# Performance work log

Measured on AMD Instinct MI355X. Metric: run time of the kernel, lower is better.

## Reference

```python
import jax, jax.numpy as jnp
import numpy as np

B, MBITS, P = 4096, 64, 64
BLK = P // 8          # 8: block size for crop-robust pattern
FREQ = P // 4         # 16: low-res frequency pattern size
KS, SIGMA = 5, 1.0


def _interp_matrix(n_in, n_out):
    # 1D bilinear interpolation matrix with align_corners=True semantics
    pos = jnp.arange(n_out, dtype=jnp.float32) * (n_in - 1) / (n_out - 1)
    lo = jnp.floor(pos).astype(jnp.int32)
    hi = jnp.minimum(lo + 1, n_in - 1)
    w = pos - lo.astype(jnp.float32)
    rows = jnp.arange(n_out)
    M = jnp.zeros((n_out, n_in), jnp.float32)
    M = M.at[rows, lo].add(1.0 - w).at[rows, hi].add(w)
    return M


def _gaussian_kernel(ks, sigma):
    c = jnp.arange(ks, dtype=jnp.float32) - ks // 2
    g = jnp.exp(-c**2 / (2.0 * sigma**2))
    g = g / g.sum()
    k2 = jnp.outer(g, g)
    return k2 / k2.sum()


def setup_inputs() -> dict:
    key = jax.random.key(0)
    ks = jax.random.split(key, 8)

    def lin(k, fan_in, fan_out):
        lim = 1.0 / np.sqrt(fan_in)
        return jax.random.uniform(k, (fan_in, fan_out), jnp.float32, -lim, lim)

    return {
        'message': jax.random.uniform(ks[0], (B, MBITS), jnp.float32),
        'sW1': lin(ks[1], MBITS, 256), 'sb1': jnp.zeros((256,), jnp.float32),
        'sW2': lin(ks[2], 256, 512),   'sb2': jnp.zeros((512,), jnp.float32),
        'sW3': lin(ks[3], 512, P * P), 'sb3': jnp.zeros((P * P,), jnp.float32),
        'fW1': lin(ks[4], MBITS, 128), 'fb1': jnp.zeros((128,), jnp.float32),
        'fW2': lin(ks[5], 128, FREQ * FREQ), 'fb2': jnp.zeros((FREQ * FREQ,), jnp.float32),
    }


def reference(message, sW1, sb1, sW2, sb2, sW3, sb3, fW1, fb1, fW2, fb2):
    b = message.shape[0]
    # --- spatial pattern: MLP -> tanh -> [B,1,P,P]
    h = jax.nn.relu(message @ sW1 + sb1)
    h = jax.nn.relu(h @ sW2 + sb2)
    spatial = jnp.tanh(h @ sW3 + sb3).reshape(b, 1, P, P)

    # --- frequency pattern: MLP -> tanh -> [B,1,16,16] -> bilinear upsample to PxP
    f = jax.nn.relu(message @ fW1 + fb1)
    freq_lo = jnp.tanh(f @ fW2 + fb2).reshape(b, FREQ, FREQ)
    M = _interp_matrix(FREQ, P)  # [P, FREQ]
    freq = jnp.einsum('ph,bhw,qw->bpq', M, freq_lo, M)[:, None]  # [B,1,P,P]

    # --- block pattern: bit i -> 8x8 block (row-major over an 8x8 grid)
    blocks = message.reshape(b, 8, 8)  # [B, rows, cols] of bits
    block = jnp.repeat(jnp.repeat(blocks, BLK, axis=1), BLK, axis=2)[:, None]  # [B,1,P,P]

    rgb = jnp.concatenate([spatial, freq, block], axis=1)  # [B,3,P,P]

    # --- depthwise 5x5 Gaussian smoothing, groups=3
    k2 = _gaussian_kernel(KS, SIGMA)
    kernel = jnp.broadcast_to(k2, (3, 1, KS, KS))
    out = jax.lax.conv_general_dilated(
        rgb, kernel, window_strides=(1, 1), padding=[(KS // 2, KS // 2)] * 2,
        dimension_numbers=('NCHW', 'OIHW', 'NCHW'), feature_group_count=3)
    return out
```

## Files before the change

kernel.cpp:

```cpp
#include <hip/hip_runtime.h>
#include <math.h>

#define BATCH 4096

typedef __attribute__((ext_vector_type(8))) short short8;
typedef __attribute__((ext_vector_type(4))) float f32x4;

__device__ __forceinline__ unsigned short f2bf(float f) {
  unsigned int u = __float_as_uint(f);
  u += 0x7FFF + ((u >> 16) & 1);
  return (unsigned short)(u >> 16);
}

__device__ __forceinline__ float bf2f(unsigned short s) {
  return __uint_as_float(((unsigned int)s) << 16);
}

__device__ __forceinline__ float fast_tanh(float x) {
  const float e = __expf(2.0f * x);
  const float r = __builtin_amdgcn_rcpf(e + 1.0f);
  return fmaf(-2.0f, r, 1.0f);
}

#define GLL16(g, l)                                                    \
  __builtin_amdgcn_global_load_lds(                                    \
      (const __attribute__((address_space(1))) unsigned int*)(g),      \
      (__attribute__((address_space(3))) unsigned int*)(l), 16, 0, 0)

__global__ __launch_bounds__(256) void prep_kernel(
    const float* __restrict__ sW1, const float* __restrict__ sW2,
    const float* __restrict__ sW3, const float* __restrict__ msg,
    unsigned short* __restrict__ w1T, unsigned short* __restrict__ w2T,
    unsigned short* __restrict__ w3T, unsigned short* __restrict__ msgb) {
  const int b = blockIdx.x;
  const int t = threadIdx.x;

  if (b >= 2192) {
    const int i0 = (b - 2192) * 2048 + t * 8;
    const float4 v0 = *reinterpret_cast<const float4*>(&msg[i0]);
    const float4 v1 = *reinterpret_cast<const float4*>(&msg[i0 + 4]);
    short8 o;
    o[0] = (short)f2bf(v0.x); o[1] = (short)f2bf(v0.y);
    o[2] = (short)f2bf(v0.z); o[3] = (short)f2bf(v0.w);
    o[4] = (short)f2bf(v1.x); o[5] = (short)f2bf(v1.y);
    o[6] = (short)f2bf(v1.z); o[7] = (short)f2bf(v1.w);
    *reinterpret_cast<short8*>(&msgb[i0]) = o;
    return;
  }

  const float* src;
  unsigned short* dst;
  int K, N, lgtN, tile;
  if (b < 16) {
    src = sW1; dst = w1T; K = 64; N = 256; lgtN = 3; tile = b;
  } else if (b < 144) {
    src = sW2; dst = w2T; K = 256; N = 512; lgtN = 4; tile = b - 16;
  } else {
    src = sW3; dst = w3T; K = 512; N = 4096; lgtN = 7; tile = b - 144;
  }
  const int ty = tile >> lgtN;
  const int tx = tile & ((1 << lgtN) - 1);

  __shared__ float tl[32][33];
  {
    const int r = t >> 3, c4 = (t & 7) * 4;
    const float4 v =
        *reinterpret_cast<const float4*>(&src[(size_t)(ty * 32 + r) * N + tx * 32 + c4]);
    tl[r][c4 + 0] = v.x; tl[r][c4 + 1] = v.y;
    tl[r][c4 + 2] = v.z; tl[r][c4 + 3] = v.w;
  }
  __syncthreads();
  {
    const int nl = t >> 3, k4 = (t & 7) * 4;
    unsigned short o[4];
#pragma unroll
    for (int i = 0; i < 4; ++i) o[i] = f2bf(tl[k4 + i][nl]);
    *reinterpret_cast<ushort4*>(&dst[(size_t)(tx * 32 + nl) * K + ty * 32 + k4]) =
        *reinterpret_cast<const ushort4*>(o);
  }
}

template <int ACT, int OBF16, int KDIM>
__global__ __launch_bounds__(256) void gemm_mfma(
    const unsigned short* __restrict__ A, const unsigned short* __restrict__ BT,
    const float* __restrict__ bias, void* __restrict__ Cv, int ldc) {
  __shared__ __align__(16) unsigned short As[128 * 32];
  __shared__ __align__(16) unsigned short Bs[128 * 32];

  const int t = threadIdx.x;
  const int lane = t & 63;
  const int w = t >> 6;
  const int bm = blockIdx.x * 128;
  const int bn = blockIdx.y * 128;

  const int r0 = w * 32 + (lane >> 2);
  const int r1 = r0 + 16;
  const int c0 = (lane & 3) ^ ((r0 >> 1) & 3);
  const int c1 = (lane & 3) ^ ((r1 >> 1) & 3);

  const unsigned short* gA0 = A + (size_t)(bm + r0) * KDIM + c0 * 8;
  const unsigned short* gA1 = A + (size_t)(bm + r1) * KDIM + c1 * 8;
  const unsigned short* gB0 = BT + (size_t)(bn + r0) * KDIM + c0 * 8;
  const unsigned short* gB1 = BT + (size_t)(bn + r1) * KDIM + c1 * 8;

  unsigned short* lA0 = &As[(w * 2 + 0) * 512];
  unsigned short* lA1 = &As[(w * 2 + 1) * 512];
  unsigned short* lB0 = &Bs[(w * 2 + 0) * 512];
  unsigned short* lB1 = &Bs[(w * 2 + 1) * 512];

  const int wm = (w >> 1) * 64;
  const int wn = (w & 1) * 64;
  const int lr = lane & 15;
  const int lc = lane >> 4;
  int aoff[4], boff[4];
#pragma unroll
  for (int i = 0; i < 4; ++i) {
    const int row = wm + i * 16 + lr;
    aoff[i] = row * 32 + (lc ^ ((row >> 1) & 3)) * 8;
    const int col = wn + i * 16 + lr;
    boff[i] = col * 32 + (lc ^ ((col >> 1) & 3)) * 8;
  }

  f32x4 acc[4][4];
  const f32x4 z = {0.f, 0.f, 0.f, 0.f};
#pragma unroll
  for (int i = 0; i < 4; ++i)
#pragma unroll
    for (int j = 0; j < 4; ++j) acc[i][j] = z;

#pragma unroll 1
  for (int kt = 0; kt < KDIM / 32; ++kt) {
    GLL16(gA0, lA0);
    GLL16(gA1, lA1);
    GLL16(gB0, lB0);
    GLL16(gB1, lB1);
    __syncthreads();

    short8 a[4], b[4];
#pragma unroll
    for (int i = 0; i < 4; ++i) a[i] = *reinterpret_cast<const short8*>(&As[aoff[i]]);
#pragma unroll
    for (int j = 0; j < 4; ++j) b[j] = *reinterpret_cast<const short8*>(&Bs[boff[j]]);

#pragma unroll
    for (int i = 0; i < 4; ++i)
#pragma unroll
      for (int j = 0; j < 4; ++j)
        acc[i][j] =
            __builtin_amdgcn_mfma_f32_16x16x32_bf16(a[i], b[j], acc[i][j], 0, 0, 0);

    __syncthreads();
    gA0 += 32; gA1 += 32; gB0 += 32; gB1 += 32;
  }

  const int base_row = bm + wm + (lc << 2);
  const int base_col = bn + wn + lr;
#pragma unroll
  for (int i = 0; i < 4; ++i) {
#pragma unroll
    for (int j = 0; j < 4; ++j) {
      const int n = base_col + j * 16;
      const float bv = bias[n];
#pragma unroll
      for (int r = 0; r < 4; ++r) {
        const int m = base_row + i * 16 + r;
        float v = acc[i][j][r] + bv;
        v = (ACT == 0) ? fmaxf(v, 0.0f) : fast_tanh(v);
        if (OBF16)
          ((unsigned short*)Cv)[(size_t)m * ldc + n] = f2bf(v);
        else
          ((float*)Cv)[(size_t)m * ldc + n] = v;
      }
    }
  }
}

__global__ __launch_bounds__(256) void freq_mlp(
    const float* __restrict__ msg, const float* __restrict__ fW1,
    const float* __restrict__ fb1, const float* __restrict__ fW2,
    const float* __restrict__ fb2, float* __restrict__ fl) {
  const int row0 = blockIdx.x * 16;
  const int t = threadIdx.x;

  __shared__ float ms[16 * 64];
  __shared__ float f1[16][128];

  *reinterpret_cast<float4*>(&ms[t * 4]) =
      *reinterpret_cast<const float4*>(&msg[(size_t)row0 * 64 + t * 4]);
  __syncthreads();

  {
    const int n = t & 127;
    const int rb = (t >> 7) * 8;
    float acc[8] = {};
    for (int k = 0; k < 64; ++k) {
      const float wv = fW1[k * 128 + n];
#pragma unroll
      for (int r = 0; r < 8; ++r) acc[r] += ms[(rb + r) * 64 + k] * wv;
    }
    const float bv = fb1[n];
#pragma unroll
    for (int r = 0; r < 8; ++r) f1[rb + r][n] = fmaxf(acc[r] + bv, 0.0f);
  }
  __syncthreads();

  {
    float acc[16] = {};
    for (int k = 0; k < 128; ++k) {
      const float wv = fW2[k * 256 + t];
#pragma unroll
      for (int r = 0; r < 16; ++r) acc[r] += f1[r][k] * wv;
    }
    const float bv = fb2[t];
#pragma unroll
    for (int r = 0; r < 16; ++r)
      fl[(size_t)(row0 + r) * 256 + t] = fast_tanh(acc[r] + bv);
  }
}

__global__ __launch_bounds__(256) void finalize_kernel(
    const float* __restrict__ msg, const float* __restrict__ fl_in,
    const unsigned short* __restrict__ spatial, float* __restrict__ out) {
  const int b = blockIdx.x;
  const int c = blockIdx.y;
  const int t = threadIdx.x;

  __shared__ float chan[4096];
  __shared__ float tmp[4096];
  __shared__ float fl[256];
  __shared__ float msgs[64];
  __shared__ int lo_tab[64];
  __shared__ float w_tab[64];

  const float g0 = 0.054488684549644346f;
  const float g1 = 0.24420134200323332f;
  const float g2 = 0.4026199468907953f;
  const float g[5] = {g0, g1, g2, g1, g0};

  if (c != 0) {
    if (t < 64) {
      msgs[t] = msg[(size_t)b * 64 + t];
      const float pos = (float)t * (15.0f / 63.0f);
      int lo = (int)floorf(pos);
      if (lo > 15) lo = 15;
      lo_tab[t] = lo;
      w_tab[t] = pos - (float)lo;
    }
    fl[t] = fl_in[(size_t)b * 256 + t];
  }
  __syncthreads();

  if (c == 0) {
    const short8* sp = reinterpret_cast<const short8*>(spatial + (size_t)b * 4096);
    for (int v = t; v < 512; v += 256) {
      const short8 s = sp[v];
#pragma unroll
      for (int j = 0; j < 8; ++j) chan[v * 8 + j] = bf2f((unsigned short)s[j]);
    }
  } else if (c == 1) {
    for (int i = t; i < 4096; i += 256) {
      const int p = i >> 6, q = i & 63;
      const int lp = lo_tab[p], lq = lo_tab[q];
      const int hp = lp < 15 ? lp + 1 : 15;
      const int hq = lq < 15 ? lq + 1 : 15;
      const float wp = w_tab[p], wq = w_tab[q];
      const float v00 = fl[lp * 16 + lq], v01 = fl[lp * 16 + hq];
      const float v10 = fl[hp * 16 + lq], v11 = fl[hp * 16 + hq];
      chan[i] = (1.0f - wp) * ((1.0f - wq) * v00 + wq * v01) +
                wp * ((1.0f - wq) * v10 + wq * v11);
    }
  } else {
    for (int i = t; i < 4096; i += 256) {
      const int p = i >> 6, q = i & 63;
      chan[i] = msgs[((p >> 3) << 3) + (q >> 3)];
    }
  }
  __syncthreads();

  for (int i = t; i < 4096; i += 256) {
    const int p = i >> 6, q = i & 63;
    float s = 0.0f;
#pragma unroll
    for (int d = -2; d <= 2; ++d) {
      const int qq = q + d;
      if (qq >= 0 && qq < 64) s += g[d + 2] * chan[p * 64 + qq];
    }
    tmp[i] = s;
  }
  __syncthreads();

  float4* dst = reinterpret_cast<float4*>(out + (size_t)b * 12288 + (size_t)c * 4096);
  for (int i = t; i < 1024; i += 256) {
    const int p = i >> 4;
    const int q4 = (i & 15) * 4;
    float s0 = 0.f, s1 = 0.f, s2 = 0.f, s3 = 0.f;
#pragma unroll
    for (int d = -2; d <= 2; ++d) {
      const int pp = p + d;
      if (pp >= 0 && pp < 64) {
        const float gg = g[d + 2];
        const int base = pp * 64 + q4;
        s0 += gg * tmp[base + 0];
        s1 += gg * tmp[base + 1];
        s2 += gg * tmp[base + 2];
        s3 += gg * tmp[base + 3];
      }
    }
    float4 v;
    v.x = s0; v.y = s1; v.z = s2; v.w = s3;
    dst[i] = v;
  }
}

extern "C" void kernel_launch(void* const* d_in, const int* in_sizes, int n_in,
                              void* d_out, int out_size, void* d_ws,
                              size_t ws_size, hipStream_t stream) {
  const float* msg = (const float*)d_in[0];
  const float* sW1 = (const float*)d_in[1];
  const float* sb1 = (const float*)d_in[2];
  const float* sW2 = (const float*)d_in[3];
  const float* sb2 = (const float*)d_in[4];
  const float* sW3 = (const float*)d_in[5];
  const float* sb3 = (const float*)d_in[6];
  const float* fW1 = (const float*)d_in[7];
  const float* fb1 = (const float*)d_in[8];
  const float* fW2 = (const float*)d_in[9];
  const float* fb2 = (const float*)d_in[10];

  float* out = (float*)d_out;
  char* wsb = (char*)d_ws;

  unsigned short* msgb = (unsigned short*)(wsb);
  unsigned short* w1T  = (unsigned short*)(wsb + (1 << 19));
  unsigned short* w2T  = (unsigned short*)(wsb + (1 << 20));
  unsigned short* w3T  = (unsigned short*)(wsb + (2 << 20));
  unsigned short* h1   = (unsigned short*)(wsb + (8 << 20));
  unsigned short* h2   = (unsigned short*)(wsb + (12 << 20));
  unsigned short* spat = (unsigned short*)(wsb + (16 << 20));
  float* fl            = (float*)(wsb + (48 << 20));

  const dim3 blk(256);

  prep_kernel<<<dim3(2320), blk, 0, stream>>>(sW1, sW2, sW3, msg, w1T, w2T, w3T, msgb);

  gemm_mfma<0, 1, 64><<<dim3(32, 2), blk, 0, stream>>>(msgb, w1T, sb1, h1, 256);
  gemm_mfma<0, 1, 256><<<dim3(32, 4), blk, 0, stream>>>(h1, w2T, sb2, h2, 512);
  gemm_mfma<1, 1, 512><<<dim3(32, 32), blk, 0, stream>>>(h2, w3T, sb3, spat, 4096);

  freq_mlp<<<dim3(256), blk, 0, stream>>>(msg, fW1, fb1, fW2, fb2, fl);

  finalize_kernel<<<dim3(BATCH, 3), blk, 0, stream>>>(msg, fl, spat, out);
}
```

Baseline: 345.2 us.

## Double GEMM K-tile to 64 and remap workgroups across XCDs

The MFMA GEMM now stages a 64-wide K slice per iteration with an 8-way XOR LDS swizzle. This halves the number of barrier-synchronised loop trips. Workgroup IDs are also remapped so that neighbouring tiles land on the same XCD, which should improve L2 reuse of the shared A/B panels. LDS use doubles to 32KB per block, which may reduce occupancy.

```diff
diff --git a/kernel.cpp b/kernel.cpp
--- a/kernel.cpp
+++ b/kernel.cpp
@@ -80,45 +80,51 @@
   }
 }
 
-template <int ACT, int OBF16, int KDIM>
+template <int ACT, int OBF16, int KDIM, int NWG>
 __global__ __launch_bounds__(256) void gemm_mfma(
     const unsigned short* __restrict__ A, const unsigned short* __restrict__ BT,
     const float* __restrict__ bias, void* __restrict__ Cv, int ldc) {
-  __shared__ __align__(16) unsigned short As[128 * 32];
-  __shared__ __align__(16) unsigned short Bs[128 * 32];
+  __shared__ __align__(16) unsigned short As[128 * 64];
+  __shared__ __align__(16) unsigned short Bs[128 * 64];
 
   const int t = threadIdx.x;
   const int lane = t & 63;
   const int w = t >> 6;
-  const int bm = blockIdx.x * 128;
-  const int bn = blockIdx.y * 128;
-
-  const int r0 = w * 32 + (lane >> 2);
-  const int r1 = r0 + 16;
-  const int c0 = (lane & 3) ^ ((r0 >> 1) & 3);
-  const int c1 = (lane & 3) ^ ((r1 >> 1) & 3);
-
-  const unsigned short* gA0 = A + (size_t)(bm + r0) * KDIM + c0 * 8;
-  const unsigned short* gA1 = A + (size_t)(bm + r1) * KDIM + c1 * 8;
-  const unsigned short* gB0 = BT + (size_t)(bn + r0) * KDIM + c0 * 8;
-  const unsigned short* gB1 = BT + (size_t)(bn + r1) * KDIM + c1 * 8;
-
-  unsigned short* lA0 = &As[(w * 2 + 0) * 512];
-  unsigned short* lA1 = &As[(w * 2 + 1) * 512];
-  unsigned short* lB0 = &Bs[(w * 2 + 0) * 512];
-  unsigned short* lB1 = &Bs[(w * 2 + 1) * 512];
+
+  const int orig = blockIdx.y * 32 + blockIdx.x;
+  const int swz = (orig & 7) * (NWG >> 3) + (orig >> 3);
+  const int bm = (swz & 31) * 128;
+  const int bn = (swz >> 5) * 128;
+
+  const int lrow = lane >> 3;
+  const int lchunk = (lane & 7) ^ lrow;
+  const unsigned short* gA[4];
+  const unsigned short* gB[4];
+  unsigned short* lA[4];
+  unsigned short* lB[4];
+#pragma unroll
+  for (int q = 0; q < 4; ++q) {
+    const int R0 = (w * 4 + q) * 8;
+    gA[q] = A + (size_t)(bm + R0 + lrow) * KDIM + lchunk * 8;
+    gB[q] = BT + (size_t)(bn + R0 + lrow) * KDIM + lchunk * 8;
+    lA[q] = &As[(w * 4 + q) * 512];
+    lB[q] = &Bs[(w * 4 + q) * 512];
+  }
 
   const int wm = (w >> 1) * 64;
   const int wn = (w & 1) * 64;
   const int lr = lane & 15;
   const int lc = lane >> 4;
-  int aoff[4], boff[4];
-#pragma unroll
-  for (int i = 0; i < 4; ++i) {
-    const int row = wm + i * 16 + lr;
-    aoff[i] = row * 32 + (lc ^ ((row >> 1) & 3)) * 8;
-    const int col = wn + i * 16 + lr;
-    boff[i] = col * 32 + (lc ^ ((col >> 1) & 3)) * 8;
+  int aoff[2][4], boff[2][4];
+#pragma unroll
+  for (int kk = 0; kk < 2; ++kk) {
+#pragma unroll
+    for (int i = 0; i < 4; ++i) {
+      const int arow = wm + i * 16 + lr;
+      aoff[kk][i] = arow * 64 + ((kk * 4 + lc) ^ (arow & 7)) * 8;
+      const int brow = wn + i * 16 + lr;
+      boff[kk][i] = brow * 64 + ((kk * 4 + lc) ^ (brow & 7)) * 8;
+    }
   }
 
   f32x4 acc[4][4];
@@ -129,28 +135,33 @@
     for (int j = 0; j < 4; ++j) acc[i][j] = z;
 
 #pragma unroll 1
-  for (int kt = 0; kt < KDIM / 32; ++kt) {
-    GLL16(gA0, lA0);
-    GLL16(gA1, lA1);
-    GLL16(gB0, lB0);
-    GLL16(gB1, lB1);
+  for (int kt = 0; kt < KDIM / 64; ++kt) {
+#pragma unroll
+    for (int q = 0; q < 4; ++q) GLL16(gA[q], lA[q]);
+#pragma unroll
+    for (int q = 0; q < 4; ++q) GLL16(gB[q], lB[q]);
     __syncthreads();
 
-    short8 a[4], b[4];
-#pragma unroll
-    for (int i = 0; i < 4; ++i) a[i] = *reinterpret_cast<const short8*>(&As[aoff[i]]);
-#pragma unroll
-    for (int j = 0; j < 4; ++j) b[j] = *reinterpret_cast<const short8*>(&Bs[boff[j]]);
-
-#pragma unroll
-    for (int i = 0; i < 4; ++i)
+#pragma unroll
+    for (int kk = 0; kk < 2; ++kk) {
+      short8 a[4], b[4];
+#pragma unroll
+      for (int i = 0; i < 4; ++i)
+        a[i] = *reinterpret_cast<const short8*>(&As[aoff[kk][i]]);
 #pragma unroll
       for (int j = 0; j < 4; ++j)
-        acc[i][j] =
-            __builtin_amdgcn_mfma_f32_16x16x32_bf16(a[i], b[j], acc[i][j], 0, 0, 0);
+        b[j] = *reinterpret_cast<const short8*>(&Bs[boff[kk][j]]);
+#pragma unroll
+      for (int i = 0; i < 4; ++i)
+#pragma unroll
+        for (int j = 0; j < 4; ++j)
+          acc[i][j] =
+              __builtin_amdgcn_mfma_f32_16x16x32_bf16(a[i], b[j], acc[i][j], 0, 0, 0);
+    }
 
     __syncthreads();
-    gA0 += 32; gA1 += 32; gB0 += 32; gB1 += 32;
+#pragma unroll
+    for (int q = 0; q < 4; ++q) { gA[q] += 64; gB[q] += 64; }
   }
 
   const int base_row = bm + wm + (lc << 2);
@@ -343,9 +354,9 @@
 
   prep_kernel<<<dim3(2320), blk, 0, stream>>>(sW1, sW2, sW3, msg, w1T, w2T, w3T, msgb);
 
-  gemm_mfma<0, 1, 64><<<dim3(32, 2), blk, 0, stream>>>(msgb, w1T, sb1, h1, 256);
-  gemm_mfma<0, 1, 256><<<dim3(32, 4), blk, 0, stream>>>(h1, w2T, sb2, h2, 512);
-  gemm_mfma<1, 1, 512><<<dim3(32, 32), blk, 0, stream>>>(h2, w3T, sb3, spat, 4096);
+  gemm_mfma<0, 1, 64, 64><<<dim3(32, 2), blk, 0, stream>>>(msgb, w1T, sb1, h1, 256);
+  gemm_mfma<0, 1, 256, 128><<<dim3(32, 4), blk, 0, stream>>>(h1, w2T, sb2, h2, 512);
+  gemm_mfma<1, 1, 512, 1024><<<dim3(32, 32), blk, 0, stream>>>(h2, w3T, sb3, spat, 4096);
 
   freq_mlp<<<dim3(256), blk, 0, stream>>>(msg, fW1, fb1, fW2, fb2, fl);
 
```

New measurement: 341.0 us. About the same (-1.2%).
